# Performance work log

Measured on AMD Instinct MI355X. Metric: run time of the kernel, lower is better.

## Reference

```python
import jax, jax.numpy as jnp
import numpy as np

EPS = 1e-12  # matches torch F.normalize default eps

def setup_inputs() -> dict:
    key = jax.random.key(0)
    x = jax.random.normal(key, (8192, 512), dtype=jnp.float32)
    return {"x": x}

def reference(x) -> jnp.ndarray:
    # q = k = v = x, shape [B, C]
    # cosine-similarity scores: L2-normalize rows, then QK^T -> [B, B]
    norm = jnp.maximum(jnp.linalg.norm(x, axis=-1, keepdims=True), EPS)
    xn = x / norm
    attn = xn @ xn.T                      # [B, B] cosine similarities
    attn = jax.nn.softmax(attn, axis=-1)  # row softmax
    out = attn @ x                        # [B, C]
    return out
```

## Files before the change

kernel.cpp:

```cpp
#include <hip/hip_runtime.h>

#define NB 8192
#define ND 512
#define QB 64
#define KB 32
#define NTILES (NB / KB)
#define TILE_BYTES (KB * ND * 2)

typedef unsigned short u16;
typedef unsigned int u32;
typedef __attribute__((ext_vector_type(8))) short bf16x8;
typedef __attribute__((ext_vector_type(4))) float f32x4;

__device__ inline u16 f2bf(float f) {
  u32 u = __float_as_uint(f);
  return (u16)((u + 0x7fffu + ((u >> 16) & 1u)) >> 16);
}

__global__ __launch_bounds__(256) void prep_norms(const float* __restrict__ x,
                                                  float* __restrict__ norms) {
  int row = blockIdx.x * 4 + (threadIdx.x >> 6);
  int lane = threadIdx.x & 63;
  const float4* xr = reinterpret_cast<const float4*>(x + (size_t)row * ND);
  float4 a = xr[lane];
  float4 b = xr[64 + lane];
  float ss = a.x * a.x + a.y * a.y + a.z * a.z + a.w * a.w +
             b.x * b.x + b.y * b.y + b.z * b.z + b.w * b.w;
  ss += __shfl_xor(ss, 1);  ss += __shfl_xor(ss, 2);  ss += __shfl_xor(ss, 4);
  ss += __shfl_xor(ss, 8);  ss += __shfl_xor(ss, 16); ss += __shfl_xor(ss, 32);
  if (lane == 0) norms[row] = 1.0f / fmaxf(sqrtf(ss), 1e-12f);
}

__global__ __launch_bounds__(256) void prep_images(const float* __restrict__ x,
                                                   u16* __restrict__ Kimg,
                                                   u16* __restrict__ Vimg) {
  __shared__ u16 Lt[TILE_BYTES / 2];
  const int t = blockIdx.x;
  const int tid = threadIdx.x;

  {
    int kv = tid >> 3, d0 = (tid & 7) * 64;
    const float* src = x + (size_t)(t * KB + kv) * ND + d0;
    char* kbase = (char*)Kimg + (size_t)t * TILE_BYTES;
#pragma unroll
    for (int j = 0; j < 8; ++j) {
      float4 f0 = *(const float4*)(src + j * 8);
      float4 f1 = *(const float4*)(src + j * 8 + 4);
      union { u16 u[8]; uint4 v; } pk;
      pk.u[0] = f2bf(f0.x); pk.u[1] = f2bf(f0.y); pk.u[2] = f2bf(f0.z); pk.u[3] = f2bf(f0.w);
      pk.u[4] = f2bf(f1.x); pk.u[5] = f2bf(f1.y); pk.u[6] = f2bf(f1.z); pk.u[7] = f2bf(f1.w);
      int byte = (kv * 1024 + (d0 + j * 8) * 2) ^ ((kv & 7) << 4);
      *(uint4*)(kbase + byte) = pk.v;
      *(uint4*)((char*)Lt + byte) = pk.v;
    }
  }
  __syncthreads();
  {
    char* vbase = (char*)Vimg + (size_t)t * TILE_BYTES;
#pragma unroll
    for (int i = 0; i < 8; ++i) {
      int gid = tid + 256 * i;
      int d = gid >> 2, kv0 = (gid & 3) * 8;
      union { u16 u[8]; uint4 v; } o;
#pragma unroll
      for (int k = 0; k < 8; ++k) {
        int sb = ((kv0 + k) * 1024 + d * 2) ^ (((kv0 + k) & 7) << 4);
        o.u[k] = *(const u16*)((const char*)Lt + sb);
      }
      int byte = (d * 64 + kv0 * 2) ^ ((d & 7) << 4);
      *(uint4*)(vbase + byte) = o.v;
    }
  }
}

template <int NCH>
__global__ __launch_bounds__(512, 2) void attn_kernel(const float* __restrict__ x,
                                                      const u16* __restrict__ Kimg,
                                                      const u16* __restrict__ Vimg,
                                                      const float* __restrict__ norms,
                                                      float* __restrict__ Opart,
                                                      float* __restrict__ Zpart,
                                                      float* __restrict__ out) {
  __shared__ u16 Kl[2][TILE_BYTES / 2];
  __shared__ u16 Vl[2][TILE_BYTES / 2];
  __shared__ u16 Pl[QB * KB];
  __shared__ float Zred[8 * 16];
  __shared__ float Zfin[QB];

  const int tid = threadIdx.x;
  const int w = tid >> 6;
  const int l = tid & 63;
  const int bid = blockIdx.x;

  int chunk, qblk;
  if constexpr (NCH == 2) {
    chunk = (bid >> 2) & 1;
    qblk = (bid & 3) * 32 + (bid >> 3);
  } else {
    chunk = 0;
    qblk = (bid & 7) * 16 + (bid >> 3);
  }
  const int CT = NTILES / NCH;
  const int tile0 = chunk * CT;

  const int qt = w & 3;
  const int kvt = w >> 2;

  bf16x8 qf[16];
  {
    int qrow = qblk * QB + qt * 16 + (l & 15);
    float rnq = norms[qrow];
    const float* xr = x + (size_t)qrow * ND;
#pragma unroll
    for (int ks = 0; ks < 16; ++ks) {
      int d0 = ks * 32 + (l >> 4) * 8;
      float4 f0 = *(const float4*)(xr + d0);
      float4 f1 = *(const float4*)(xr + d0 + 4);
      union { u16 u[8]; bf16x8 v; } pk;
      pk.u[0] = f2bf(f0.x * rnq); pk.u[1] = f2bf(f0.y * rnq);
      pk.u[2] = f2bf(f0.z * rnq); pk.u[3] = f2bf(f0.w * rnq);
      pk.u[4] = f2bf(f1.x * rnq); pk.u[5] = f2bf(f1.y * rnq);
      pk.u[6] = f2bf(f1.z * rnq); pk.u[7] = f2bf(f1.w * rnq);
      qf[ks] = pk.v;
    }
  }

  auto stage = [&](int tg, int b) {
    size_t toff = (size_t)tg * TILE_BYTES;
#pragma unroll
    for (int j = 0; j < 4; ++j) {
      const char* src = (const char*)Kimg + toff + (w * 4 + j) * 1024 + l * 16;
      char* dst = (char*)&Kl[b][0] + (w * 4 + j) * 1024;
      __builtin_amdgcn_global_load_lds((const void*)src, (void*)dst, 16, 0, 0);
    }
#pragma unroll
    for (int j = 0; j < 4; ++j) {
      const char* src = (const char*)Vimg + toff + (w * 4 + j) * 1024 + l * 16;
      char* dst = (char*)&Vl[b][0] + (w * 4 + j) * 1024;
      __builtin_amdgcn_global_load_lds((const void*)src, (void*)dst, 16, 0, 0);
    }
  };

  stage(tile0, 0);

  f32x4 oacc[4][4];
#pragma unroll
  for (int a = 0; a < 4; ++a)
#pragma unroll
    for (int b = 0; b < 4; ++b) oacc[a][b] = (f32x4){0.f, 0.f, 0.f, 0.f};
  float zacc = 0.f;

  const int kv = kvt * 16 + (l & 15);
  const int rowbase = kv * 1024;
  const int kswz = (kv & 7) << 4;
  const int hi16 = (l >> 4) * 16;

  for (int t = 0; t < CT; ++t) {
    const int buf = t & 1;
    asm volatile("s_waitcnt vmcnt(0)" ::: "memory");
    __builtin_amdgcn_s_barrier();
    __builtin_amdgcn_sched_barrier(0);
    if (t + 1 < CT) stage(tile0 + t + 1, buf ^ 1);

    f32x4 acc0 = {0.f, 0.f, 0.f, 0.f}, acc1 = {0.f, 0.f, 0.f, 0.f};
    {
      const char* kb = (const char*)&Kl[buf][0];
#pragma unroll
      for (int ks = 0; ks < 16; ks += 2) {
        bf16x8 k0 = *(const bf16x8*)(kb + ((rowbase + ks * 64 + hi16) ^ kswz));
        bf16x8 k1 = *(const bf16x8*)(kb + ((rowbase + (ks + 1) * 64 + hi16) ^ kswz));
        acc0 = __builtin_amdgcn_mfma_f32_16x16x32_bf16(k0, qf[ks], acc0, 0, 0, 0);
        acc1 = __builtin_amdgcn_mfma_f32_16x16x32_bf16(k1, qf[ks + 1], acc1, 0, 0, 0);
      }
    }
    {
      int kvbase = kvt * 16 + (l >> 4) * 4;
      float4 rn4 = *(const float4*)(norms + (tile0 + t) * KB + kvbase);
      float p0 = __expf((acc0[0] + acc1[0]) * rn4.x);
      float p1 = __expf((acc0[1] + acc1[1]) * rn4.y);
      float p2 = __expf((acc0[2] + acc1[2]) * rn4.z);
      float p3 = __expf((acc0[3] + acc1[3]) * rn4.w);
      zacc += (p0 + p1) + (p2 + p3);
      u32 w01, w23;
      asm("v_cvt_pk_bf16_f32 %0, %1, %2" : "=v"(w01) : "v"(p0), "v"(p1));
      asm("v_cvt_pk_bf16_f32 %0, %1, %2" : "=v"(w23) : "v"(p2), "v"(p3));
      int q = qt * 16 + (l & 15);
      int pbyte = ((q * KB + kvbase) * 2) ^ ((q & 7) << 4);
      *(uint2*)((char*)Pl + pbyte) = (uint2){w01, w23};
    }
    asm volatile("s_waitcnt lgkmcnt(0)" ::: "memory");
    __builtin_amdgcn_s_barrier();
    __builtin_amdgcn_sched_barrier(0);

    {
      const char* plb = (const char*)Pl;
      bf16x8 pa[4];
#pragma unroll
      for (int q2 = 0; q2 < 4; ++q2) {
        int qr = q2 * 16 + (l & 15);
        pa[q2] = *(const bf16x8*)(plb + (((qr * KB) * 2 + hi16) ^ ((qr & 7) << 4)));
      }
      const char* vb = (const char*)&Vl[buf][0];
#pragma unroll
      for (int dt = 0; dt < 4; ++dt) {
        int d = w * 64 + dt * 16 + (l & 15);
        bf16x8 vf = *(const bf16x8*)(vb + ((d * 64 + hi16) ^ ((d & 7) << 4)));
#pragma unroll
        for (int q2 = 0; q2 < 4; ++q2)
          oacc[q2][dt] =
              __builtin_amdgcn_mfma_f32_16x16x32_bf16(pa[q2], vf, oacc[q2][dt], 0, 0, 0);
      }
    }
  }

  {
    float s = zacc;
    s += __shfl_xor(s, 16);
    s += __shfl_xor(s, 32);
    if (l < 16) Zred[w * 16 + l] = s;
  }
  __syncthreads();

  if constexpr (NCH == 2) {
    if (tid < QB) {
      int qt_ = tid >> 4;
      float z = Zred[qt_ * 16 + (tid & 15)] + Zred[(qt_ + 4) * 16 + (tid & 15)];
      Zpart[chunk * NB + qblk * QB + tid] = z;
    }
    float* op = Opart + (size_t)chunk * NB * ND;
#pragma unroll
    for (int q2 = 0; q2 < 4; ++q2)
#pragma unroll
      for (int dt = 0; dt < 4; ++dt) {
        int d = w * 64 + dt * 16 + (l & 15);
#pragma unroll
        for (int r = 0; r < 4; ++r) {
          int q = qblk * QB + q2 * 16 + (l >> 4) * 4 + r;
          op[(size_t)q * ND + d] = oacc[q2][dt][r];
        }
      }
  } else {
    if (tid < QB) {
      int qt_ = tid >> 4;
      Zfin[tid] = Zred[qt_ * 16 + (tid & 15)] + Zred[(qt_ + 4) * 16 + (tid & 15)];
    }
    __syncthreads();
#pragma unroll
    for (int q2 = 0; q2 < 4; ++q2) {
      float rz[4];
#pragma unroll
      for (int r = 0; r < 4; ++r) rz[r] = 1.0f / Zfin[q2 * 16 + (l >> 4) * 4 + r];
#pragma unroll
      for (int dt = 0; dt < 4; ++dt) {
        int d = w * 64 + dt * 16 + (l & 15);
#pragma unroll
        for (int r = 0; r < 4; ++r) {
          int q = qblk * QB + q2 * 16 + (l >> 4) * 4 + r;
          out[(size_t)q * ND + d] = oacc[q2][dt][r] * rz[r];
        }
      }
    }
  }
}

__global__ __launch_bounds__(256) void combine_kernel(const float* __restrict__ Opart,
                                                      const float* __restrict__ Zpart,
                                                      float* __restrict__ out) {
  size_t idx = ((size_t)blockIdx.x * 256 + threadIdx.x) * 4;
  int row = (int)(idx >> 9);
  float rz = 1.0f / (Zpart[row] + Zpart[NB + row]);
  float4 a = *(const float4*)(Opart + idx);
  float4 b = *(const float4*)(Opart + (size_t)NB * ND + idx);
  float4 o = {(a.x + b.x) * rz, (a.y + b.y) * rz, (a.z + b.z) * rz, (a.w + b.w) * rz};
  *(float4*)(out + idx) = o;
}

extern "C" void kernel_launch(void* const* d_in, const int* in_sizes, int n_in,
                              void* d_out, int out_size, void* d_ws, size_t ws_size,
                              hipStream_t stream) {
  const float* x = (const float*)d_in[0];
  float* outp = (float*)d_out;

  char* ws = (char*)d_ws;
  const size_t img_bytes = (size_t)NB * ND * 2;
  float* norms = (float*)ws;
  u16* Kimg = (u16*)(ws + 32768);
  u16* Vimg = (u16*)(ws + 32768 + img_bytes);
  size_t base = 32768 + 2 * img_bytes;
  float* Zpart = (float*)(ws + base);
  float* Opart = (float*)(ws + base + 65536);
  size_t need = base + 65536 + (size_t)2 * NB * ND * 4;

  prep_norms<<<NB / 4, 256, 0, stream>>>(x, norms);
  prep_images<<<NTILES, 256, 0, stream>>>(x, Kimg, Vimg);
  if (ws_size >= need) {
    attn_kernel<2><<<256, 512, 0, stream>>>(x, Kimg, Vimg, norms, Opart, Zpart, nullptr);
    combine_kernel<<<(NB * ND) / 1024, 256, 0, stream>>>(Opart, Zpart, outp);
  } else {
    attn_kernel<1><<<128, 512, 0, stream>>>(x, Kimg, Vimg, norms, nullptr, nullptr, outp);
  }
}
```

Measured before the change: 272.3 us.

## Widen KV tile to 64 and split K/V staging into single-buffered phases

Doubles the key/value tile from 32 to 64 rows and drops the double-buffered LDS for K and V in favour of single buffers. Loading is split so the next K tile is fetched during the P·V phase and the next V tile during the QK phase. Each wave now computes two query subtiles against one 16-row KV slice, and the partial row sums are reduced across four KV groups. The aim is fewer barriers per key and more MFMA work per barrier at the same LDS footprint, at the cost of less lookahead, since each load now has only one phase to complete in.

```diff
diff --git a/kernel.cpp b/kernel.cpp
--- a/kernel.cpp
+++ b/kernel.cpp
@@ -3,7 +3,7 @@
 #define NB 8192
 #define ND 512
 #define QB 64
-#define KB 32
+#define KB 64
 #define NTILES (NB / KB)
 #define TILE_BYTES (KB * ND * 2)
 
@@ -34,16 +34,16 @@
 __global__ __launch_bounds__(256) void prep_images(const float* __restrict__ x,
                                                    u16* __restrict__ Kimg,
                                                    u16* __restrict__ Vimg) {
-  __shared__ u16 Lt[TILE_BYTES / 2];
+  __shared__ u16 Lt[KB * ND];
   const int t = blockIdx.x;
   const int tid = threadIdx.x;
 
   {
-    int kv = tid >> 3, d0 = (tid & 7) * 64;
+    int kv = tid >> 2, d0 = (tid & 3) * 128;
     const float* src = x + (size_t)(t * KB + kv) * ND + d0;
     char* kbase = (char*)Kimg + (size_t)t * TILE_BYTES;
 #pragma unroll
-    for (int j = 0; j < 8; ++j) {
+    for (int j = 0; j < 16; ++j) {
       float4 f0 = *(const float4*)(src + j * 8);
       float4 f1 = *(const float4*)(src + j * 8 + 4);
       union { u16 u[8]; uint4 v; } pk;
@@ -58,16 +58,16 @@
   {
     char* vbase = (char*)Vimg + (size_t)t * TILE_BYTES;
 #pragma unroll
-    for (int i = 0; i < 8; ++i) {
+    for (int i = 0; i < 16; ++i) {
       int gid = tid + 256 * i;
-      int d = gid >> 2, kv0 = (gid & 3) * 8;
+      int d = gid >> 3, kv0 = (gid & 7) * 8;
       union { u16 u[8]; uint4 v; } o;
 #pragma unroll
       for (int k = 0; k < 8; ++k) {
         int sb = ((kv0 + k) * 1024 + d * 2) ^ (((kv0 + k) & 7) << 4);
         o.u[k] = *(const u16*)((const char*)Lt + sb);
       }
-      int byte = (d * 64 + kv0 * 2) ^ ((d & 7) << 4);
+      int byte = (d * 128 + kv0 * 2) ^ ((d & 7) << 4);
       *(uint4*)(vbase + byte) = o.v;
     }
   }
@@ -81,10 +81,10 @@
                                                       float* __restrict__ Opart,
                                                       float* __restrict__ Zpart,
                                                       float* __restrict__ out) {
-  __shared__ u16 Kl[2][TILE_BYTES / 2];
-  __shared__ u16 Vl[2][TILE_BYTES / 2];
+  __shared__ u16 Kl[KB * ND];
+  __shared__ u16 Vl[KB * ND];
   __shared__ u16 Pl[QB * KB];
-  __shared__ float Zred[8 * 16];
+  __shared__ float Zred[256];
   __shared__ float Zfin[QB];
 
   const int tid = threadIdx.x;
@@ -101,14 +101,16 @@
     qblk = (bid & 7) * 16 + (bid >> 3);
   }
   const int CT = NTILES / NCH;
+  const int CHUNK = NB / NCH;
   const int tile0 = chunk * CT;
 
-  const int qt = w & 3;
-  const int kvt = w >> 2;
-
-  bf16x8 qf[16];
-  {
-    int qrow = qblk * QB + qt * 16 + (l & 15);
+  const int pq = w & 1;
+  const int tkv = w >> 1;
+
+  bf16x8 qf[2][16];
+#pragma unroll
+  for (int a = 0; a < 2; ++a) {
+    int qrow = qblk * QB + (pq * 2 + a) * 16 + (l & 15);
     float rnq = norms[qrow];
     const float* xr = x + (size_t)qrow * ND;
 #pragma unroll
@@ -121,111 +123,132 @@
       pk.u[2] = f2bf(f0.z * rnq); pk.u[3] = f2bf(f0.w * rnq);
       pk.u[4] = f2bf(f1.x * rnq); pk.u[5] = f2bf(f1.y * rnq);
       pk.u[6] = f2bf(f1.z * rnq); pk.u[7] = f2bf(f1.w * rnq);
-      qf[ks] = pk.v;
-    }
-  }
-
-  auto stage = [&](int tg, int b) {
+      qf[a][ks] = pk.v;
+    }
+  }
+
+  auto stageK = [&](int tg) {
     size_t toff = (size_t)tg * TILE_BYTES;
 #pragma unroll
-    for (int j = 0; j < 4; ++j) {
-      const char* src = (const char*)Kimg + toff + (w * 4 + j) * 1024 + l * 16;
-      char* dst = (char*)&Kl[b][0] + (w * 4 + j) * 1024;
+    for (int j = 0; j < 8; ++j) {
+      const char* src = (const char*)Kimg + toff + (w * 8 + j) * 1024 + l * 16;
+      char* dst = (char*)Kl + (w * 8 + j) * 1024;
       __builtin_amdgcn_global_load_lds((const void*)src, (void*)dst, 16, 0, 0);
     }
-#pragma unroll
-    for (int j = 0; j < 4; ++j) {
-      const char* src = (const char*)Vimg + toff + (w * 4 + j) * 1024 + l * 16;
-      char* dst = (char*)&Vl[b][0] + (w * 4 + j) * 1024;
+  };
+  auto stageV = [&](int tg) {
+    size_t toff = (size_t)tg * TILE_BYTES;
+#pragma unroll
+    for (int j = 0; j < 8; ++j) {
+      const char* src = (const char*)Vimg + toff + (w * 8 + j) * 1024 + l * 16;
+      char* dst = (char*)Vl + (w * 8 + j) * 1024;
       __builtin_amdgcn_global_load_lds((const void*)src, (void*)dst, 16, 0, 0);
     }
   };
 
-  stage(tile0, 0);
+  stageK(tile0);
+  asm volatile("s_waitcnt vmcnt(0)" ::: "memory");
+  __builtin_amdgcn_s_barrier();
+  __builtin_amdgcn_sched_barrier(0);
+  stageV(tile0);
 
   f32x4 oacc[4][4];
 #pragma unroll
   for (int a = 0; a < 4; ++a)
 #pragma unroll
     for (int b = 0; b < 4; ++b) oacc[a][b] = (f32x4){0.f, 0.f, 0.f, 0.f};
-  float zacc = 0.f;
-
-  const int kv = kvt * 16 + (l & 15);
-  const int rowbase = kv * 1024;
+  float za[2] = {0.f, 0.f};
+
+  const int kv = tkv * 16 + (l & 15);
+  const int krowbase = kv * 1024;
   const int kswz = (kv & 7) << 4;
   const int hi16 = (l >> 4) * 16;
 
   for (int t = 0; t < CT; ++t) {
-    const int buf = t & 1;
-    asm volatile("s_waitcnt vmcnt(0)" ::: "memory");
+    f32x4 acc0 = {0.f, 0.f, 0.f, 0.f}, acc1 = {0.f, 0.f, 0.f, 0.f};
+    {
+      const char* kb = (const char*)Kl;
+#pragma unroll
+      for (int ks = 0; ks < 16; ++ks) {
+        bf16x8 kf = *(const bf16x8*)(kb + ((krowbase + ks * 64 + hi16) ^ kswz));
+        acc0 = __builtin_amdgcn_mfma_f32_16x16x32_bf16(kf, qf[0][ks], acc0, 0, 0, 0);
+        acc1 = __builtin_amdgcn_mfma_f32_16x16x32_bf16(kf, qf[1][ks], acc1, 0, 0, 0);
+      }
+    }
+    {
+      int kvb = tkv * 16 + (l >> 4) * 4;
+      float4 rn4 = *(const float4*)(norms + chunk * CHUNK + t * KB + kvb);
+#pragma unroll
+      for (int a = 0; a < 2; ++a) {
+        const f32x4& ac = a ? acc1 : acc0;
+        float p0 = __expf(ac[0] * rn4.x);
+        float p1 = __expf(ac[1] * rn4.y);
+        float p2 = __expf(ac[2] * rn4.z);
+        float p3 = __expf(ac[3] * rn4.w);
+        za[a] += (p0 + p1) + (p2 + p3);
+        u32 w01, w23;
+        asm("v_cvt_pk_bf16_f32 %0, %1, %2" : "=v"(w01) : "v"(p0), "v"(p1));
+        asm("v_cvt_pk_bf16_f32 %0, %1, %2" : "=v"(w23) : "v"(p2), "v"(p3));
+        int q = (pq * 2 + a) * 16 + (l & 15);
+        int pbyte = (q * 128 + kvb * 2) ^ ((q & 7) << 4);
+        *(uint2*)((char*)Pl + pbyte) = (uint2){w01, w23};
+      }
+    }
+    asm volatile("s_waitcnt vmcnt(0) lgkmcnt(0)" ::: "memory");
     __builtin_amdgcn_s_barrier();
     __builtin_amdgcn_sched_barrier(0);
-    if (t + 1 < CT) stage(tile0 + t + 1, buf ^ 1);
-
-    f32x4 acc0 = {0.f, 0.f, 0.f, 0.f}, acc1 = {0.f, 0.f, 0.f, 0.f};
+    if (t + 1 < CT) stageK(tile0 + t + 1);
+
     {
-      const char* kb = (const char*)&Kl[buf][0];
-#pragma unroll
-      for (int ks = 0; ks < 16; ks += 2) {
-        bf16x8 k0 = *(const bf16x8*)(kb + ((rowbase + ks * 64 + hi16) ^ kswz));
-        bf16x8 k1 = *(const bf16x8*)(kb + ((rowbase + (ks + 1) * 64 + hi16) ^ kswz));
-        acc0 = __builtin_amdgcn_mfma_f32_16x16x32_bf16(k0, qf[ks], acc0, 0, 0, 0);
-        acc1 = __builtin_amdgcn_mfma_f32_16x16x32_bf16(k1, qf[ks + 1], acc1, 0, 0, 0);
-      }
-    }
-    {
-      int kvbase = kvt * 16 + (l >> 4) * 4;
-      float4 rn4 = *(const float4*)(norms + (tile0 + t) * KB + kvbase);
-      float p0 = __expf((acc0[0] + acc1[0]) * rn4.x);
-      float p1 = __expf((acc0[1] + acc1[1]) * rn4.y);
-      float p2 = __expf((acc0[2] + acc1[2]) * rn4.z);
-      float p3 = __expf((acc0[3] + acc1[3]) * rn4.w);
-      zacc += (p0 + p1) + (p2 + p3);
-      u32 w01, w23;
-      asm("v_cvt_pk_bf16_f32 %0, %1, %2" : "=v"(w01) : "v"(p0), "v"(p1));
-      asm("v_cvt_pk_bf16_f32 %0, %1, %2" : "=v"(w23) : "v"(p2), "v"(p3));
-      int q = qt * 16 + (l & 15);
-      int pbyte = ((q * KB + kvbase) * 2) ^ ((q & 7) << 4);
-      *(uint2*)((char*)Pl + pbyte) = (uint2){w01, w23};
-    }
-    asm volatile("s_waitcnt lgkmcnt(0)" ::: "memory");
+      const char* plb = (const char*)Pl;
+      bf16x8 pa[4][2];
+#pragma unroll
+      for (int q2 = 0; q2 < 4; ++q2) {
+        int qr = q2 * 16 + (l & 15);
+        int qswz = (qr & 7) << 4;
+#pragma unroll
+        for (int ks = 0; ks < 2; ++ks)
+          pa[q2][ks] = *(const bf16x8*)(plb + ((qr * 128 + ks * 64 + hi16) ^ qswz));
+      }
+      const char* vb = (const char*)Vl;
+#pragma unroll
+      for (int dt = 0; dt < 4; ++dt) {
+        int d = w * 64 + dt * 16 + (l & 15);
+        int vswz = (d & 7) << 4;
+#pragma unroll
+        for (int ks = 0; ks < 2; ++ks) {
+          bf16x8 vf = *(const bf16x8*)(vb + ((d * 128 + ks * 64 + hi16) ^ vswz));
+#pragma unroll
+          for (int q2 = 0; q2 < 4; ++q2)
+            oacc[q2][dt] =
+                __builtin_amdgcn_mfma_f32_16x16x32_bf16(pa[q2][ks], vf, oacc[q2][dt], 0, 0, 0);
+        }
+      }
+    }
+    asm volatile("s_waitcnt vmcnt(0) lgkmcnt(0)" ::: "memory");
     __builtin_amdgcn_s_barrier();
     __builtin_amdgcn_sched_barrier(0);
-
-    {
-      const char* plb = (const char*)Pl;
-      bf16x8 pa[4];
-#pragma unroll
-      for (int q2 = 0; q2 < 4; ++q2) {
-        int qr = q2 * 16 + (l & 15);
-        pa[q2] = *(const bf16x8*)(plb + (((qr * KB) * 2 + hi16) ^ ((qr & 7) << 4)));
-      }
-      const char* vb = (const char*)&Vl[buf][0];
-#pragma unroll
-      for (int dt = 0; dt < 4; ++dt) {
-        int d = w * 64 + dt * 16 + (l & 15);
-        bf16x8 vf = *(const bf16x8*)(vb + ((d * 64 + hi16) ^ ((d & 7) << 4)));
-#pragma unroll
-        for (int q2 = 0; q2 < 4; ++q2)
-          oacc[q2][dt] =
-              __builtin_amdgcn_mfma_f32_16x16x32_bf16(pa[q2], vf, oacc[q2][dt], 0, 0, 0);
-      }
-    }
+    if (t + 1 < CT) stageV(tile0 + t + 1);
   }
 
   {
-    float s = zacc;
-    s += __shfl_xor(s, 16);
-    s += __shfl_xor(s, 32);
-    if (l < 16) Zred[w * 16 + l] = s;
+#pragma unroll
+    for (int a = 0; a < 2; ++a) {
+      float s = za[a];
+      s += __shfl_xor(s, 16);
+      s += __shfl_xor(s, 32);
+      if (l < 16) Zred[w * 32 + a * 16 + l] = s;
+    }
   }
   __syncthreads();
 
   if constexpr (NCH == 2) {
     if (tid < QB) {
-      int qt_ = tid >> 4;
-      float z = Zred[qt_ * 16 + (tid & 15)] + Zred[(qt_ + 4) * 16 + (tid & 15)];
-      Zpart[chunk * NB + qblk * QB + tid] = z;
+      int g = tid >> 4, p_ = g >> 1, a_ = g & 1;
+      float s = 0.f;
+#pragma unroll
+      for (int tk = 0; tk < 4; ++tk) s += Zred[(tk * 2 + p_) * 32 + a_ * 16 + (tid & 15)];
+      Zpart[chunk * NB + qblk * QB + tid] = s;
     }
     float* op = Opart + (size_t)chunk * NB * ND;
 #pragma unroll
@@ -241,8 +264,11 @@
       }
   } else {
     if (tid < QB) {
-      int qt_ = tid >> 4;
-      Zfin[tid] = Zred[qt_ * 16 + (tid & 15)] + Zred[(qt_ + 4) * 16 + (tid & 15)];
+      int g = tid >> 4, p_ = g >> 1, a_ = g & 1;
+      float s = 0.f;
+#pragma unroll
+      for (int tk = 0; tk < 4; ++tk) s += Zred[(tk * 2 + p_) * 32 + a_ * 16 + (tid & 15)];
+      Zfin[tid] = s;
     }
     __syncthreads();
 #pragma unroll
```

Result: slower. 299.0 us (+9.8%).
